# Performance work log

Measured on AMD Instinct MI355X. Metric: run time of the kernel, lower is better.

## Reference

```python
import jax, jax.numpy as jnp
import numpy as np

B, S, D, H = 4, 1024, 1024, 16
DH = D // H  # per-head dim


def setup_inputs() -> dict:
    key = jax.random.key(0)
    ks = jax.random.split(key, 9)
    f = lambda k, sh: jax.random.normal(k, sh, dtype=jnp.float32)
    return {
        "query": f(ks[0], (B, S, D)),
        "key": f(ks[1], (B, S, D)),
        "value": f(ks[2], (B, S, D)),
        "mask": jax.random.randint(ks[3], (B, S), 0, 2).astype(jnp.int32),
        "pos_emb": f(ks[4], (H, S, DH)),
        "W_q": f(ks[5], (D, D)) * 0.02,
        "W_k": f(ks[6], (D, D)) * 0.02,
        "W_v": f(ks[7], (D, D)) * 0.02,
        "W_o": f(ks[8], (D, D)) * 0.02,
    }


def _shift(x):
    """Music-Transformer skew trick. x: [b,h,i,j] -> [b,h,i,j]."""
    b, h, i, j = x.shape
    x = jnp.concatenate([x, jnp.zeros((b, h, i, i), x.dtype)], axis=-1)  # [b,h,i,i+j]
    l = i + j - 1
    flat = x.reshape(b, h, i * (i + j))
    pad = (-flat.shape[-1]) % l
    flat = jnp.concatenate([flat, jnp.zeros((b, h, pad), flat.dtype)], axis=-1)
    return flat.reshape(b, h, -1, l)[:, :, :i, i - 1:]


def reference(query, key, value, mask, pos_emb, W_q, W_k, W_v, W_o):
    b, s, _ = query.shape
    # torch Linear(bias=False): y = x @ W.T ; then split heads -> [b,h,s,dh]
    proj = lambda x, W: (x @ W.T).reshape(b, s, H, DH).transpose(0, 2, 1, 3)
    q = proj(query, W_q)
    k = proj(key, W_k)
    v = proj(value, W_v)

    dots = jnp.einsum('bhid,bhjd->bhij', q, k) * (DH ** -0.5)
    pe = pos_emb[:, :s, :]  # [h,s,dh]
    # NOTE: original code scales positional scores by dim ** (+0.5)
    pos_dots = jnp.einsum('bhid,hjd->bhij', q, pe) * (DH ** 0.5)
    dots = dots + _shift(pos_dots)

    m = (mask[:, :, None] * mask[:, None, :])[:, None]  # [b,1,s,s]
    dots = jnp.where(m == 0, jnp.float32(-1e9), dots)

    attn = jax.nn.softmax(dots, axis=-1)  # dropout omitted (eval / p=0)
    x = jnp.einsum('bhij,bhjd->bhid', attn, v)
    x = x.transpose(0, 2, 1, 3).reshape(b, s, H * DH)
    return x @ W_o.T
```

## Files before the change

kernel.cpp:

```cpp
#include <hip/hip_runtime.h>
#include <math.h>

#define BB 4
#define SS 1024
#define DD 1024
#define HH 16
#define DHH 64

typedef _Float16 half8 __attribute__((ext_vector_type(8)));
typedef _Float16 half4v __attribute__((ext_vector_type(4)));
typedef float v4f __attribute__((ext_vector_type(4)));
typedef unsigned int u32;
typedef unsigned short u16;

__device__ __forceinline__ void gload_lds16(const void* g, void* l) {
    __builtin_amdgcn_global_load_lds(
        (const __attribute__((address_space(1))) u32*)(const u32*)g,
        (__attribute__((address_space(3))) u32*)(u32*)l, 16, 0, 0);
}

__global__ __launch_bounds__(256) void convert_kernel(
    const float* __restrict__ wq, const float* __restrict__ wk,
    const float* __restrict__ wv, const float* __restrict__ wo,
    const float* __restrict__ pe, _Float16* __restrict__ dst)
{
    const int i4 = blockIdx.x * 256 + threadIdx.x;
    const int region = i4 >> 18;
    const int local4 = i4 & 262143;
    const float* srcs[5] = {wq, wk, wv, wo, pe};
    const float scales[5] = {1.0f, 0.125f, 1.0f, 1.0f, 8.0f};
    const float sc = scales[region];
    float4 v = *(const float4*)(srcs[region] + (size_t)local4 * 4);
    half4v h = {(_Float16)(v.x * sc), (_Float16)(v.y * sc),
                (_Float16)(v.z * sc), (_Float16)(v.w * sc)};
    *(half4v*)(dst + ((size_t)region << 20) + (size_t)local4 * 4) = h;
}

__global__ __launch_bounds__(256) void gemm_proj(
    const float* __restrict__ Aq, const float* __restrict__ Ak,
    const float* __restrict__ Av,
    const _Float16* __restrict__ Wqf, const _Float16* __restrict__ Wkf,
    const _Float16* __restrict__ Wvf,
    _Float16* __restrict__ Cq, _Float16* __restrict__ Ck,
    _Float16* __restrict__ Cv)
{
    __shared__ _Float16 As[128 * 32];
    __shared__ _Float16 Bs[64 * 32];

    const int z = blockIdx.z;
    const float* A = z == 0 ? Aq : z == 1 ? Ak : Av;
    const _Float16* W = z == 0 ? Wqf : z == 1 ? Wkf : Wvf;
    _Float16* C = z == 0 ? Cq : z == 1 ? Ck : Cv;

    const int tid = threadIdx.x;
    const int w = tid >> 6, lane = tid & 63, lm = lane & 15, quad = lane >> 4;
    const int n0 = blockIdx.x * 64, m0 = blockIdx.y * 128;

    const int brow = tid >> 2, blc = (tid & 3) ^ (brow & 3);

    v4f zero4 = {0.f, 0.f, 0.f, 0.f};
    v4f acc[2][4];
#pragma unroll
    for (int mi = 0; mi < 2; mi++)
#pragma unroll
        for (int ni = 0; ni < 4; ni++) acc[mi][ni] = zero4;

    for (int k0 = 0; k0 < DD; k0 += 32) {
        __syncthreads();
        gload_lds16(W + (size_t)(n0 + brow) * DD + k0 + blc * 8, Bs + tid * 8);
#pragma unroll
        for (int u = 0; u < 4; u++) {
            int c4 = tid + 256 * u;
            int row = c4 >> 3, k4 = c4 & 7;
            float4 v = *(const float4*)(A + (size_t)(m0 + row) * DD + k0 + k4 * 4);
            half4v hv = {(_Float16)v.x, (_Float16)v.y, (_Float16)v.z, (_Float16)v.w};
            int c16 = k4 >> 1, hlf = k4 & 1;
            *(half4v*)(As + row * 32 + (((c16 ^ (row & 3)) << 3) + (hlf << 2))) = hv;
        }
        __syncthreads();

        half8 af[2], bf[4];
#pragma unroll
        for (int mi = 0; mi < 2; mi++) {
            int row = w * 32 + mi * 16 + lm;
            af[mi] = *(const half8*)(As + row * 32 + ((quad ^ (row & 3)) << 3));
        }
#pragma unroll
        for (int ni = 0; ni < 4; ni++) {
            int row = ni * 16 + lm;
            bf[ni] = *(const half8*)(Bs + row * 32 + ((quad ^ (row & 3)) << 3));
        }
#pragma unroll
        for (int mi = 0; mi < 2; mi++)
#pragma unroll
            for (int ni = 0; ni < 4; ni++)
                acc[mi][ni] = __builtin_amdgcn_mfma_f32_16x16x32_f16(
                    af[mi], bf[ni], acc[mi][ni], 0, 0, 0);
    }

    const int h = n0 >> 6;
#pragma unroll
    for (int mi = 0; mi < 2; mi++)
#pragma unroll
        for (int r = 0; r < 4; r++) {
            int m = m0 + w * 32 + mi * 16 + quad * 4 + r;
            int b = m >> 10, s = m & 1023;
            size_t base = ((size_t)(b * HH + h) * SS + s) * DHH;
#pragma unroll
            for (int ni = 0; ni < 4; ni++)
                C[base + ni * 16 + lm] = (_Float16)acc[mi][ni][r];
        }
}

__global__ __launch_bounds__(256) void gemm_out(
    const _Float16* __restrict__ A, const _Float16* __restrict__ W,
    float* __restrict__ C)
{
    __shared__ _Float16 As[128 * 32];
    __shared__ _Float16 Bs[64 * 32];

    const int tid = threadIdx.x;
    const int w = tid >> 6, lane = tid & 63, lm = lane & 15, quad = lane >> 4;
    const int n0 = blockIdx.x * 64, m0 = blockIdx.y * 128;
    const int brow = tid >> 2, blc = (tid & 3) ^ (brow & 3);

    v4f zero4 = {0.f, 0.f, 0.f, 0.f};
    v4f acc[2][4];
#pragma unroll
    for (int mi = 0; mi < 2; mi++)
#pragma unroll
        for (int ni = 0; ni < 4; ni++) acc[mi][ni] = zero4;

    for (int k0 = 0; k0 < DD; k0 += 32) {
        __syncthreads();
        gload_lds16(W + (size_t)(n0 + brow) * DD + k0 + blc * 8, Bs + tid * 8);
#pragma unroll
        for (int u = 0; u < 2; u++) {
            int p = tid + 256 * u;
            int row = p >> 2, lc = (p & 3) ^ (row & 3);
            gload_lds16(A + (size_t)(m0 + row) * DD + k0 + lc * 8, As + p * 8);
        }
        __syncthreads();

        half8 af[2], bf[4];
#pragma unroll
        for (int mi = 0; mi < 2; mi++) {
            int row = w * 32 + mi * 16 + lm;
            af[mi] = *(const half8*)(As + row * 32 + ((quad ^ (row & 3)) << 3));
        }
#pragma unroll
        for (int ni = 0; ni < 4; ni++) {
            int row = ni * 16 + lm;
            bf[ni] = *(const half8*)(Bs + row * 32 + ((quad ^ (row & 3)) << 3));
        }
#pragma unroll
        for (int mi = 0; mi < 2; mi++)
#pragma unroll
            for (int ni = 0; ni < 4; ni++)
                acc[mi][ni] = __builtin_amdgcn_mfma_f32_16x16x32_f16(
                    af[mi], bf[ni], acc[mi][ni], 0, 0, 0);
    }

#pragma unroll
    for (int mi = 0; mi < 2; mi++)
#pragma unroll
        for (int r = 0; r < 4; r++) {
            size_t base = (size_t)(m0 + w * 32 + mi * 16 + quad * 4 + r) * DD
                        + n0 + lm;
#pragma unroll
            for (int ni = 0; ni < 4; ni++)
                C[base + ni * 16] = acc[mi][ni][r];
        }
}

__global__ __launch_bounds__(256) void attn_mfma(
    const _Float16* __restrict__ Qg, const _Float16* __restrict__ Kg,
    const _Float16* __restrict__ Vg, const int* __restrict__ mask,
    const _Float16* __restrict__ peg, _Float16* __restrict__ Og)
{
    __shared__ _Float16 Ks[64 * 72];
    __shared__ _Float16 Vt[64 * 72];
    __shared__ _Float16 PEb[128 * 72];
    __shared__ _Float16 Pb[4][16 * 72];

    const int tid = threadIdx.x;
    const int w = tid >> 6, lane = tid & 63;
    const int lm = lane & 15, quad = lane >> 4;
    const int it = blockIdx.x, i0 = it * 64;
    const int bh = blockIdx.y, b = bh >> 4, h = bh & 15;

    const _Float16* Qb = Qg + (size_t)bh * SS * DHH;
    const _Float16* Kb = Kg + (size_t)bh * SS * DHH;
    const _Float16* Vb = Vg + (size_t)bh * SS * DHH;
    const _Float16* peh = peg + (size_t)h * SS * DHH;

    float mi_f[4];
#pragma unroll
    for (int r = 0; r < 4; r++)
        mi_f[r] = (float)mask[b * SS + i0 + w * 16 + quad * 4 + r];

    half8 qf[2];
#pragma unroll
    for (int kc = 0; kc < 2; kc++)
        qf[kc] = *(const half8*)(Qb + (size_t)(i0 + w * 16 + lm) * DHH
                                 + kc * 32 + quad * 8);

    const int srow = tid >> 3, sk8 = tid & 7;

    v4f zero4 = {0.f, 0.f, 0.f, 0.f};
    float m_run[4], l_run[4];
    v4f oacc[4];
#pragma unroll
    for (int r = 0; r < 4; r++) { m_run[r] = -1e30f; l_run[r] = 0.f; }
#pragma unroll
    for (int nb = 0; nb < 4; nb++) oacc[nb] = zero4;

    half8 kreg[2], vreg[2], pereg[4];
#pragma unroll
    for (int u = 0; u < 2; u++) {
        int row = srow + 32 * u;
        kreg[u] = *(const half8*)(Kb + (size_t)row * DHH + sk8 * 8);
        vreg[u] = *(const half8*)(Vb + (size_t)row * DHH + sk8 * 8);
    }
    {
        const int g0 = SS - 1 - i0 - 63;
#pragma unroll
        for (int u = 0; u < 4; u++) {
            int o = srow + 32 * u;
            int g = g0 + o;
            half8 v = {0, 0, 0, 0, 0, 0, 0, 0};
            if (g < SS) v = *(const half8*)(peh + (size_t)g * DHH + sk8 * 8);
            pereg[u] = v;
        }
    }

    for (int jt = 0; jt < SS / 64; jt++) {
        const int j0 = jt * 64;
        const bool do_pe = (jt <= it);
        __syncthreads();

#pragma unroll
        for (int u = 0; u < 2; u++) {
            int row = srow + 32 * u;
            *(half8*)(Ks + row * 72 + sk8 * 8) = kreg[u];
        }
#pragma unroll
        for (int u = 0; u < 2; u++) {
            int row = srow + 32 * u;
            int jsw = row ^ (sk8 << 3);
#pragma unroll
            for (int e = 0; e < 8; e++) Vt[(sk8 * 8 + e) * 72 + jsw] = vreg[u][e];
        }
        if (do_pe) {
#pragma unroll
            for (int u = 0; u < 4; u++) {
                int o = srow + 32 * u;
                *(half8*)(PEb + o * 72 + sk8 * 8) = pereg[u];
            }
        }
        float mj_f[4];
#pragma unroll
        for (int nb = 0; nb < 4; nb++)
            mj_f[nb] = (float)mask[b * SS + j0 + nb * 16 + lm];
        __syncthreads();

        if (jt + 1 < SS / 64) {
            const int j0n = j0 + 64;
#pragma unroll
            for (int u = 0; u < 2; u++) {
                int row = srow + 32 * u;
                kreg[u] = *(const half8*)(Kb + (size_t)(j0n + row) * DHH + sk8 * 8);
                vreg[u] = *(const half8*)(Vb + (size_t)(j0n + row) * DHH + sk8 * 8);
            }
            if (jt + 1 <= it) {
                const int g0n = SS - 1 + j0n - i0 - 63;
#pragma unroll
                for (int u = 0; u < 4; u++) {
                    int o = srow + 32 * u;
                    int g = g0n + o;
                    half8 v = {0, 0, 0, 0, 0, 0, 0, 0};
                    if (g < SS) v = *(const half8*)(peh + (size_t)g * DHH + sk8 * 8);
                    pereg[u] = v;
                }
            }
        }

        v4f sacc[4];
#pragma unroll
        for (int nb = 0; nb < 4; nb++) sacc[nb] = zero4;
        __builtin_amdgcn_s_setprio(1);
#pragma unroll
        for (int nb = 0; nb < 4; nb++)
#pragma unroll
            for (int kc = 0; kc < 2; kc++) {
                half8 kf = *(const half8*)(Ks + (nb * 16 + lm) * 72 + kc * 32 + quad * 8);
                sacc[nb] = __builtin_amdgcn_mfma_f32_16x16x32_f16(qf[kc], kf, sacc[nb], 0, 0, 0);
            }
        __builtin_amdgcn_s_setprio(0);

        if (do_pe) {
            v4f racc[5];
#pragma unroll
            for (int e = 0; e < 5; e++) racc[e] = zero4;
            __builtin_amdgcn_s_setprio(1);
#pragma unroll
            for (int e = 0; e < 5; e++) {
                int row = (e + 3 - w) * 16 + lm;
#pragma unroll
                for (int kc = 0; kc < 2; kc++) {
                    half8 pf = *(const half8*)(PEb + row * 72 + kc * 32 + quad * 8);
                    racc[e] = __builtin_amdgcn_mfma_f32_16x16x32_f16(qf[kc], pf, racc[e], 0, 0, 0);
                }
            }
            __builtin_amdgcn_s_setprio(0);
#pragma unroll
            for (int nb = 0; nb < 4; nb++)
#pragma unroll
                for (int r = 0; r < 4; r++) {
                    int qr = quad * 4 + r;
                    float vsrc = (((lm + qr + 1) & 15) <= qr)
                               ? racc[nb][r] : racc[nb + 1][r];
                    int src = (lane & 48) | ((lm - qr - 1) & 15);
                    sacc[nb][r] += __shfl(vsrc, src);
                }
        }

        float p[4][4];
        float alpha[4];
#pragma unroll
        for (int i = 0; i < 4; i++) {
            float mi = mi_f[i];
            float rmax = -1e30f;
#pragma unroll
            for (int j = 0; j < 4; j++) {
                float s = sacc[j][i];
                if (mi * mj_f[j] == 0.f) s = -1e9f;
                sacc[j][i] = s;
                rmax = fmaxf(rmax, s);
            }
#pragma unroll
            for (int off = 1; off < 16; off <<= 1)
                rmax = fmaxf(rmax, __shfl_xor(rmax, off));
            float mnew = fmaxf(m_run[i], rmax);
            alpha[i] = __expf(m_run[i] - mnew);
            m_run[i] = mnew;
            float rsum = 0.f;
#pragma unroll
            for (int j = 0; j < 4; j++) {
                p[j][i] = __expf(sacc[j][i] - mnew);
                rsum += p[j][i];
            }
#pragma unroll
            for (int off = 1; off < 16; off <<= 1)
                rsum += __shfl_xor(rsum, off);
            l_run[i] = l_run[i] * alpha[i] + rsum;
        }

        _Float16* Pw = &Pb[w][0];
#pragma unroll
        for (int nb = 0; nb < 4; nb++)
#pragma unroll
            for (int r = 0; r < 4; r++)
                Pw[(quad * 4 + r) * 72 + nb * 16 + lm] = (_Float16)p[nb][r];
#pragma unroll
        for (int nb = 0; nb < 4; nb++)
#pragma unroll
            for (int r = 0; r < 4; r++) oacc[nb][r] *= alpha[r];

        __builtin_amdgcn_s_setprio(1);
#pragma unroll
        for (int kc = 0; kc < 2; kc++) {
            half8 pfrag = *(const half8*)(Pw + lm * 72 + kc * 32 + quad * 8);
#pragma unroll
            for (int nb = 0; nb < 4; nb++) {
                int d = nb * 16 + lm;
                int col = (kc * 32 + quad * 8) ^ (((d >> 3) & 7) << 3);
                half8 vfrag = *(const half8*)(Vt + d * 72 + col);
                oacc[nb] = __builtin_amdgcn_mfma_f32_16x16x32_f16(pfrag, vfrag, oacc[nb], 0, 0, 0);
            }
        }
        __builtin_amdgcn_s_setprio(0);
    }

#pragma unroll
    for (int r = 0; r < 4; r++) {
        float inv = 1.f / l_run[r];
        int s = i0 + w * 16 + quad * 4 + r;
#pragma unroll
        for (int nb = 0; nb < 4; nb++)
            Og[((size_t)b * SS + s) * DD + h * DHH + nb * 16 + lm] =
                (_Float16)(oacc[nb][r] * inv);
    }
}

extern "C" void kernel_launch(void* const* d_in, const int* in_sizes, int n_in,
                              void* d_out, int out_size, void* d_ws, size_t ws_size,
                              hipStream_t stream)
{
    const float* query = (const float*)d_in[0];
    const float* key   = (const float*)d_in[1];
    const float* value = (const float*)d_in[2];
    const int*   mask  = (const int*)d_in[3];
    const float* pe    = (const float*)d_in[4];
    const float* Wq    = (const float*)d_in[5];
    const float* Wk    = (const float*)d_in[6];
    const float* Wv    = (const float*)d_in[7];
    const float* Wo    = (const float*)d_in[8];
    float* out = (float*)d_out;

    _Float16* ws16 = (_Float16*)d_ws;
    const size_t MEG = 1048576;
    _Float16* wqf = ws16;
    _Float16* wkf = ws16 + 1 * MEG;
    _Float16* wvf = ws16 + 2 * MEG;
    _Float16* wof = ws16 + 3 * MEG;
    _Float16* pef = ws16 + 4 * MEG;
    _Float16* qp  = ws16 + 5 * MEG;
    _Float16* kp  = ws16 + 9 * MEG;
    _Float16* vp  = ws16 + 13 * MEG;
    _Float16* ao  = ws16 + 17 * MEG;

    convert_kernel<<<5120, 256, 0, stream>>>(Wq, Wk, Wv, Wo, pe, ws16);

    gemm_proj<<<dim3(DD / 64, (BB * SS) / 128, 3), 256, 0, stream>>>(
        query, key, value, wqf, wkf, wvf, qp, kp, vp);

    attn_mfma<<<dim3(SS / 64, BB * HH), 256, 0, stream>>>(qp, kp, vp, mask, pef, ao);

    gemm_out<<<dim3(DD / 64, (BB * SS) / 128), 256, 0, stream>>>(ao, wof, out);
}
```

Measured before the change: 306.6 us.

## Pre-convert activations to fp16 for async-LDS projection GEMM; XOR-swizzle attention LDS

When enough workspace exists, a widened conversion kernel also casts query/key/value to fp16. This lets the projection GEMM load both operands straight into LDS with global_load_lds, instead of reading fp32 activations and converting them in the loop. Separately, the attention kernel drops its padded 72-stride LDS rows for 64-stride rows with an XOR swizzle, which cuts LDS footprint while avoiding bank conflicts. The cost is an extra full read/write pass over the activations and a larger workspace, with the old path kept as a fallback.

```diff
diff --git a/kernel.cpp b/kernel.cpp
--- a/kernel.cpp
+++ b/kernel.cpp
@@ -36,7 +36,33 @@
     *(half4v*)(dst + ((size_t)region << 20) + (size_t)local4 * 4) = h;
 }
 
-__global__ __launch_bounds__(256) void gemm_proj(
+__global__ __launch_bounds__(256) void convert2_kernel(
+    const float* __restrict__ wq, const float* __restrict__ wk,
+    const float* __restrict__ wv, const float* __restrict__ wo,
+    const float* __restrict__ pe, const float* __restrict__ q,
+    const float* __restrict__ k, const float* __restrict__ vv,
+    _Float16* __restrict__ dst)
+{
+    const int i4 = blockIdx.x * 256 + threadIdx.x;
+    const int region = i4 >> 18;
+    const int local4 = i4 & 262143;
+    const float* src;
+    float sc = 1.0f;
+    if (region == 0)      { src = wq; }
+    else if (region == 1) { src = wk; sc = 0.125f; }
+    else if (region == 2) { src = wv; }
+    else if (region == 3) { src = wo; }
+    else if (region == 4) { src = pe; sc = 8.0f; }
+    else if (region < 9)  { src = q  + ((size_t)(region - 5)  << 20); }
+    else if (region < 13) { src = k  + ((size_t)(region - 9)  << 20); }
+    else                  { src = vv + ((size_t)(region - 13) << 20); }
+    float4 v = *(const float4*)(src + (size_t)local4 * 4);
+    half4v h = {(_Float16)(v.x * sc), (_Float16)(v.y * sc),
+                (_Float16)(v.z * sc), (_Float16)(v.w * sc)};
+    *(half4v*)(dst + ((size_t)region << 20) + (size_t)local4 * 4) = h;
+}
+
+__global__ __launch_bounds__(256) void gemm_proj_f32(
     const float* __restrict__ Aq, const float* __restrict__ Ak,
     const float* __restrict__ Av,
     const _Float16* __restrict__ Wqf, const _Float16* __restrict__ Wkf,
@@ -112,12 +138,21 @@
         }
 }
 
-__global__ __launch_bounds__(256) void gemm_out(
-    const _Float16* __restrict__ A, const _Float16* __restrict__ W,
-    float* __restrict__ C)
+__global__ __launch_bounds__(256) void gemm_proj_f16(
+    const _Float16* __restrict__ Aq, const _Float16* __restrict__ Ak,
+    const _Float16* __restrict__ Av,
+    const _Float16* __restrict__ Wqf, const _Float16* __restrict__ Wkf,
+    const _Float16* __restrict__ Wvf,
+    _Float16* __restrict__ Cq, _Float16* __restrict__ Ck,
+    _Float16* __restrict__ Cv)
 {
     __shared__ _Float16 As[128 * 32];
     __shared__ _Float16 Bs[64 * 32];
+
+    const int z = blockIdx.z;
+    const _Float16* A = z == 0 ? Aq : z == 1 ? Ak : Av;
+    const _Float16* W = z == 0 ? Wqf : z == 1 ? Wkf : Wvf;
+    _Float16* C = z == 0 ? Cq : z == 1 ? Ck : Cv;
 
     const int tid = threadIdx.x;
     const int w = tid >> 6, lane = tid & 63, lm = lane & 15, quad = lane >> 4;
@@ -161,6 +196,69 @@
                     af[mi], bf[ni], acc[mi][ni], 0, 0, 0);
     }
 
+    const int h = n0 >> 6;
+#pragma unroll
+    for (int mi = 0; mi < 2; mi++)
+#pragma unroll
+        for (int r = 0; r < 4; r++) {
+            int m = m0 + w * 32 + mi * 16 + quad * 4 + r;
+            int b = m >> 10, s = m & 1023;
+            size_t base = ((size_t)(b * HH + h) * SS + s) * DHH;
+#pragma unroll
+            for (int ni = 0; ni < 4; ni++)
+                C[base + ni * 16 + lm] = (_Float16)acc[mi][ni][r];
+        }
+}
+
+__global__ __launch_bounds__(256) void gemm_out(
+    const _Float16* __restrict__ A, const _Float16* __restrict__ W,
+    float* __restrict__ C)
+{
+    __shared__ _Float16 As[128 * 32];
+    __shared__ _Float16 Bs[64 * 32];
+
+    const int tid = threadIdx.x;
+    const int w = tid >> 6, lane = tid & 63, lm = lane & 15, quad = lane >> 4;
+    const int n0 = blockIdx.x * 64, m0 = blockIdx.y * 128;
+    const int brow = tid >> 2, blc = (tid & 3) ^ (brow & 3);
+
+    v4f zero4 = {0.f, 0.f, 0.f, 0.f};
+    v4f acc[2][4];
+#pragma unroll
+    for (int mi = 0; mi < 2; mi++)
+#pragma unroll
+        for (int ni = 0; ni < 4; ni++) acc[mi][ni] = zero4;
+
+    for (int k0 = 0; k0 < DD; k0 += 32) {
+        __syncthreads();
+        gload_lds16(W + (size_t)(n0 + brow) * DD + k0 + blc * 8, Bs + tid * 8);
+#pragma unroll
+        for (int u = 0; u < 2; u++) {
+            int p = tid + 256 * u;
+            int row = p >> 2, lc = (p & 3) ^ (row & 3);
+            gload_lds16(A + (size_t)(m0 + row) * DD + k0 + lc * 8, As + p * 8);
+        }
+        __syncthreads();
+
+        half8 af[2], bf[4];
+#pragma unroll
+    for (int mi = 0; mi < 2; mi++) {
+            int row = w * 32 + mi * 16 + lm;
+            af[mi] = *(const half8*)(As + row * 32 + ((quad ^ (row & 3)) << 3));
+        }
+#pragma unroll
+        for (int ni = 0; ni < 4; ni++) {
+            int row = ni * 16 + lm;
+            bf[ni] = *(const half8*)(Bs + row * 32 + ((quad ^ (row & 3)) << 3));
+        }
+#pragma unroll
+        for (int mi = 0; mi < 2; mi++)
+#pragma unroll
+            for (int ni = 0; ni < 4; ni++)
+                acc[mi][ni] = __builtin_amdgcn_mfma_f32_16x16x32_f16(
+                    af[mi], bf[ni], acc[mi][ni], 0, 0, 0);
+    }
+
 #pragma unroll
     for (int mi = 0; mi < 2; mi++)
 #pragma unroll
@@ -178,10 +276,10 @@
     const _Float16* __restrict__ Vg, const int* __restrict__ mask,
     const _Float16* __restrict__ peg, _Float16* __restrict__ Og)
 {
-    __shared__ _Float16 Ks[64 * 72];
-    __shared__ _Float16 Vt[64 * 72];
-    __shared__ _Float16 PEb[128 * 72];
-    __shared__ _Float16 Pb[4][16 * 72];
+    __shared__ _Float16 Ks[64 * 64];
+    __shared__ _Float16 Vt[64 * 64];
+    __shared__ _Float16 PEb[128 * 64];
+    __shared__ _Float16 Pb[4][16 * 64];
 
     const int tid = threadIdx.x;
     const int w = tid >> 6, lane = tid & 63;
@@ -206,6 +304,7 @@
                                  + kc * 32 + quad * 8);
 
     const int srow = tid >> 3, sk8 = tid & 7;
+    const int lmx = (lm & 7) << 3;
 
     v4f zero4 = {0.f, 0.f, 0.f, 0.f};
     float m_run[4], l_run[4];
@@ -242,20 +341,20 @@
 #pragma unroll
         for (int u = 0; u < 2; u++) {
             int row = srow + 32 * u;
-            *(half8*)(Ks + row * 72 + sk8 * 8) = kreg[u];
+            *(half8*)(Ks + row * 64 + ((sk8 * 8) ^ ((row & 7) << 3))) = kreg[u];
         }
 #pragma unroll
         for (int u = 0; u < 2; u++) {
             int row = srow + 32 * u;
             int jsw = row ^ (sk8 << 3);
 #pragma unroll
-            for (int e = 0; e < 8; e++) Vt[(sk8 * 8 + e) * 72 + jsw] = vreg[u][e];
+            for (int e = 0; e < 8; e++) Vt[(sk8 * 8 + e) * 64 + jsw] = vreg[u][e];
         }
         if (do_pe) {
 #pragma unroll
             for (int u = 0; u < 4; u++) {
                 int o = srow + 32 * u;
-                *(half8*)(PEb + o * 72 + sk8 * 8) = pereg[u];
+                *(half8*)(PEb + o * 64 + ((sk8 * 8) ^ ((o & 7) << 3))) = pereg[u];
             }
         }
         float mj_f[4];
@@ -293,7 +392,8 @@
         for (int nb = 0; nb < 4; nb++)
 #pragma unroll
             for (int kc = 0; kc < 2; kc++) {
-                half8 kf = *(const half8*)(Ks + (nb * 16 + lm) * 72 + kc * 32 + quad * 8);
+                half8 kf = *(const half8*)(Ks + (nb * 16 + lm) * 64
+                                           + ((kc * 32 + quad * 8) ^ lmx));
                 sacc[nb] = __builtin_amdgcn_mfma_f32_16x16x32_f16(qf[kc], kf, sacc[nb], 0, 0, 0);
             }
         __builtin_amdgcn_s_setprio(0);
@@ -308,7 +408,8 @@
                 int row = (e + 3 - w) * 16 + lm;
 #pragma unroll
                 for (int kc = 0; kc < 2; kc++) {
-                    half8 pf = *(const half8*)(PEb + row * 72 + kc * 32 + quad * 8);
+                    half8 pf = *(const half8*)(PEb + row * 64
+                                               + ((kc * 32 + quad * 8) ^ lmx));
                     racc[e] = __builtin_amdgcn_mfma_f32_16x16x32_f16(qf[kc], pf, racc[e], 0, 0, 0);
                 }
             }
@@ -360,8 +461,10 @@
 #pragma unroll
         for (int nb = 0; nb < 4; nb++)
 #pragma unroll
-            for (int r = 0; r < 4; r++)
-                Pw[(quad * 4 + r) * 72 + nb * 16 + lm] = (_Float16)p[nb][r];
+            for (int r = 0; r < 4; r++) {
+                int qr = quad * 4 + r;
+                Pw[qr * 64 + ((nb * 16 + lm) ^ ((qr & 7) << 3))] = (_Float16)p[nb][r];
+            }
 #pragma unroll
         for (int nb = 0; nb < 4; nb++)
 #pragma unroll
@@ -370,12 +473,12 @@
         __builtin_amdgcn_s_setprio(1);
 #pragma unroll
         for (int kc = 0; kc < 2; kc++) {
-            half8 pfrag = *(const half8*)(Pw + lm * 72 + kc * 32 + quad * 8);
+            half8 pfrag = *(const half8*)(Pw + lm * 64 + ((kc * 32 + quad * 8) ^ lmx));
 #pragma unroll
             for (int nb = 0; nb < 4; nb++) {
                 int d = nb * 16 + lm;
                 int col = (kc * 32 + quad * 8) ^ (((d >> 3) & 7) << 3);
-                half8 vfrag = *(const half8*)(Vt + d * 72 + col);
+                half8 vfrag = *(const half8*)(Vt + d * 64 + col);
                 oacc[nb] = __builtin_amdgcn_mfma_f32_16x16x32_f16(pfrag, vfrag, oacc[nb], 0, 0, 0);
             }
         }
@@ -415,17 +518,42 @@
     _Float16* wvf = ws16 + 2 * MEG;
     _Float16* wof = ws16 + 3 * MEG;
     _Float16* pef = ws16 + 4 * MEG;
-    _Float16* qp  = ws16 + 5 * MEG;
-    _Float16* kp  = ws16 + 9 * MEG;
-    _Float16* vp  = ws16 + 13 * MEG;
-    _Float16* ao  = ws16 + 17 * MEG;
-
-    convert_kernel<<<5120, 256, 0, stream>>>(Wq, Wk, Wv, Wo, pe, ws16);
-
-    gemm_proj<<<dim3(DD / 64, (BB * SS) / 128, 3), 256, 0, stream>>>(
-        query, key, value, wqf, wkf, wvf, qp, kp, vp);
-
-    attn_mfma<<<dim3(SS / 64, BB * HH), 256, 0, stream>>>(qp, kp, vp, mask, pef, ao);
-
-    gemm_out<<<dim3(DD / 64, (BB * SS) / 128), 256, 0, stream>>>(ao, wof, out);
-}
+
+    const bool big = ws_size >= (size_t)33 * MEG * sizeof(_Float16);
+
+    if (big) {
+        _Float16* q16 = ws16 + 5 * MEG;
+        _Float16* k16 = ws16 + 9 * MEG;
+        _Float16* v16 = ws16 + 13 * MEG;
+        _Float16* qp  = ws16 + 17 * MEG;
+        _Float16* kp  = ws16 + 21 * MEG;
+        _Float16* vp  = ws16 + 25 * MEG;
+        _Float16* ao  = ws16 + 29 * MEG;
+
+        convert2_kernel<<<17408, 256, 0, stream>>>(
+            Wq, Wk, Wv, Wo, pe, query, key, value, ws16);
+
+        gemm_proj_f16<<<dim3(DD / 64, (BB * SS) / 128, 3), 256, 0, stream>>>(
+            q16, k16, v16, wqf, wkf, wvf, qp, kp, vp);
+
+        attn_mfma<<<dim3(SS / 64, BB * HH), 256, 0, stream>>>(
+            qp, kp, vp, mask, pef, ao);
+
+        gemm_out<<<dim3(DD / 64, (BB * SS) / 128), 256, 0, stream>>>(ao, wof, out);
+    } else {
+        _Float16* qp  = ws16 + 5 * MEG;
+        _Float16* kp  = ws16 + 9 * MEG;
+        _Float16* vp  = ws16 + 13 * MEG;
+        _Float16* ao  = ws16 + 17 * MEG;
+
+        convert_kernel<<<5120, 256, 0, stream>>>(Wq, Wk, Wv, Wo, pe, ws16);
+
+        gemm_proj_f32<<<dim3(DD / 64, (BB * SS) / 128, 3), 256, 0, stream>>>(
+            query, key, value, wqf, wkf, wvf, qp, kp, vp);
+
+        attn_mfma<<<dim3(SS / 64, BB * HH), 256, 0, stream>>>(
+            qp, kp, vp, mask, pef, ao);
+
+        gemm_out<<<dim3(DD / 64, (BB * SS) / 128), 256, 0, stream>>>(ao, wof, out);
+    }
+}
```

New measurement: 293.8 us. 4.2% less time.
